# Performance work log

Hardware: AMD Instinct MI355X
Metric: run time of the kernel (lower is better)

The kernel has to match this reference:

```python
import jax, jax.numpy as jnp
import numpy as np
from jax import lax

GAMMA = 0.99

def setup_inputs() -> dict:
    key = jax.random.key(0)
    ks = jax.random.split(key, 6)
    B, T, D = 2048, 512, 16
    return {
        "Q": jax.random.normal(ks[0], (B, T, D), dtype=jnp.float32),
        "expected_target_Q": jax.random.normal(ks[1], (B, T, D), dtype=jnp.float32),
        "target_Q": jax.random.normal(ks[2], (B, T, D), dtype=jnp.float32),
        "rewards": jax.random.normal(ks[3], (B, T, D), dtype=jnp.float32),
        "target_policy_probs": jax.random.normal(ks[4], (B, T, D), dtype=jnp.float32),
        "behaviour_policy_probs": jax.random.normal(ks[5], (B, T), dtype=jnp.float32),
    }


def _q_ret(expected_target_Q, target_Q, rewards, target_policy_probs, behaviour_policy_probs):
    # importance weights c = exp(min(log_pi - log_b, 0)), shape [B, T, D]
    c = jnp.exp(jnp.minimum(target_policy_probs - behaviour_policy_probs[..., None], 0.0))
    T = target_Q.shape[1]
    # time-major slices for steps j = 0..T-2
    tm = lambda x: jnp.swapaxes(x, 0, 1)  # [T, B, D] -> scan over leading axis
    xs = (tm(rewards[:, : T - 1]), tm(expected_target_Q[:, 1:]),
          tm(c[:, 1:]), tm(target_Q[:, 1:]))

    def step(carry, x):
        r, e, cw, tq = x
        q = r + GAMMA * (e + cw * (carry - tq))
        return q, q

    # reverse scan: Q_ret[j] depends on Q_ret[j+1]; init carry is target_Q[:, -1]
    _, q_ret = lax.scan(step, target_Q[:, -1], xs, reverse=True)
    return jnp.swapaxes(q_ret, 0, 1)  # [B, T-1, D] == Q_ret[:, :-1]


def reference(Q, expected_target_Q, target_Q, rewards, target_policy_probs, behaviour_policy_probs):
    q_ret = lax.stop_gradient(
        _q_ret(expected_target_Q, target_Q, rewards, target_policy_probs, behaviour_policy_probs))
    return jnp.mean((Q[:, :-1] - q_ret) ** 2)
```

## Files before the change

kernel.cpp:

```cpp
#include <hip/hip_runtime.h>


constexpr int B = 2048;
constexpr int T = 512;
constexpr int D = 16;
constexpr float GAMMA = 0.99f;

__global__ __launch_bounds__(64) void retrace_kernel(
    const float* __restrict__ Q,
    const float* __restrict__ eQ,
    const float* __restrict__ tQ,
    const float* __restrict__ rw,
    const float* __restrict__ tpp,
    const float* __restrict__ bpp,
    float* __restrict__ out)
{
    const int tid = blockIdx.x * blockDim.x + threadIdx.x;
    const int b = tid >> 4;
    const int d = tid & 15;

    const size_t base = (size_t)b * T * D + d;
    const float* __restrict__ q_p = Q   + base;
    const float* __restrict__ e_p = eQ  + base;
    const float* __restrict__ t_p = tQ  + base;
    const float* __restrict__ r_p = rw  + base;
    const float* __restrict__ p_p = tpp + base;
    const float* __restrict__ b_p = bpp + (size_t)b * T;

    float carry = t_p[(size_t)(T - 1) * D];
    float acc = 0.0f;

    #pragma unroll 8
    for (int j = T - 2; j >= 0; --j) {
        const float diff = p_p[(size_t)(j + 1) * D] - b_p[j + 1];
        const float cw   = __builtin_exp2f(fminf(diff, 0.0f) * 1.44269504088896340736f);
        const float tqv  = t_p[(size_t)(j + 1) * D];
        const float ev   = e_p[(size_t)(j + 1) * D];
        const float rv   = r_p[(size_t)j * D];
        const float qv   = q_p[(size_t)j * D];

        const float q = fmaf(GAMMA, fmaf(cw, carry - tqv, ev), rv);
        const float err = qv - q;
        acc = fmaf(err, err, acc);
        carry = q;
    }

    #pragma unroll
    for (int off = 32; off > 0; off >>= 1)
        acc += __shfl_down(acc, off, 64);

    if (threadIdx.x == 0) {
        constexpr float inv_count = 1.0f / ((float)B * (float)(T - 1) * (float)D);
        atomicAdd(out, acc * inv_count);
    }
}

extern "C" void kernel_launch(void* const* d_in, const int* in_sizes, int n_in,
                              void* d_out, int out_size, void* d_ws, size_t ws_size,
                              hipStream_t stream) {
    const float* Q   = (const float*)d_in[0];
    const float* eQ  = (const float*)d_in[1];
    const float* tQ  = (const float*)d_in[2];
    const float* rw  = (const float*)d_in[3];
    const float* tpp = (const float*)d_in[4];
    const float* bpp = (const float*)d_in[5];
    float* out = (float*)d_out;

    hipMemsetAsync(out, 0, sizeof(float), stream);

    retrace_kernel<<<dim3(512), dim3(64), 0, stream>>>(Q, eQ, tQ, rw, tpp, bpp, out);
}
```

Before: 333.6 us.

## Parallelize reverse scan over time chunks with affine carry composition

Splits the time axis into 16 chunks of 32 steps. Each chunk computes its affine carry map (alpha, beta) plus partial sums that make the squared-error loss a quadratic in the unknown incoming carry. A second small kernel walks the chunks in reverse, applies the carry and sums the loss exactly. Loads are widened to float4 with four features per thread. The old kernel ran only 512 wavefronts, each through a 511-step serial chain, so the GPU was badly underfilled. The cost is a workspace round trip, a second launch, and possible floating-point reassociation error from expanding the square.

```diff
diff --git a/kernel.cpp b/kernel.cpp
--- a/kernel.cpp
+++ b/kernel.cpp
@@ -4,47 +4,120 @@
 constexpr int B = 2048;
 constexpr int T = 512;
 constexpr int D = 16;
+constexpr int NC = 16;
+constexpr int CS = 32;
+constexpr int SQ = B * (D / 4);
 constexpr float GAMMA = 0.99f;
+constexpr float LOG2E = 1.44269504088896340736f;
 
-__global__ __launch_bounds__(64) void retrace_kernel(
+__global__ __launch_bounds__(256) void retrace_phase1(
     const float* __restrict__ Q,
     const float* __restrict__ eQ,
     const float* __restrict__ tQ,
     const float* __restrict__ rw,
     const float* __restrict__ tpp,
     const float* __restrict__ bpp,
+    float4* __restrict__ ws)
+{
+    const int s  = blockIdx.x * blockDim.x + threadIdx.x;
+    const int k  = blockIdx.y;
+    const int b  = s >> 2;
+    const int dq = s & 3;
+
+    const int j_start = k * CS;
+    const int j_end   = min(j_start + CS, T - 1);
+
+    const float4* __restrict__ q4 = (const float4*)Q;
+    const float4* __restrict__ e4 = (const float4*)eQ;
+    const float4* __restrict__ t4 = (const float4*)tQ;
+    const float4* __restrict__ r4 = (const float4*)rw;
+    const float4* __restrict__ p4 = (const float4*)tpp;
+    const size_t row = (size_t)b * T * 4 + dq;
+    const float* __restrict__ b_p = bpp + (size_t)b * T;
+
+    float alpha[4] = {0.f, 0.f, 0.f, 0.f};
+    float beta[4]  = {1.f, 1.f, 1.f, 1.f};
+    float P[4] = {0.f, 0.f, 0.f, 0.f};
+    float S[4] = {0.f, 0.f, 0.f, 0.f};
+    float W[4] = {0.f, 0.f, 0.f, 0.f};
+
+    #pragma unroll 4
+    for (int j = j_end - 1; j >= j_start; --j) {
+        const float4 tp4 = p4[row + (size_t)(j + 1) * 4];
+        const float4 tq4 = t4[row + (size_t)(j + 1) * 4];
+        const float4 ee4 = e4[row + (size_t)(j + 1) * 4];
+        const float4 rr4 = r4[row + (size_t)j * 4];
+        const float4 qq4 = q4[row + (size_t)j * 4];
+        const float  bp  = b_p[j + 1];
+
+        const float* tp = (const float*)&tp4;
+        const float* tq = (const float*)&tq4;
+        const float* ee = (const float*)&ee4;
+        const float* rr = (const float*)&rr4;
+        const float* qq = (const float*)&qq4;
+
+        #pragma unroll
+        for (int i = 0; i < 4; ++i) {
+            const float cw = __builtin_exp2f(fminf(tp[i] - bp, 0.f) * LOG2E);
+            const float g  = GAMMA * cw;
+            const float base = fmaf(-g, tq[i], fmaf(GAMMA, ee[i], rr[i]));
+            alpha[i] = fmaf(g, alpha[i], base);
+            beta[i]  = g * beta[i];
+            const float u = qq[i] - alpha[i];
+            P[i] = fmaf(u, u, P[i]);
+            S[i] = fmaf(u, beta[i], S[i]);
+            W[i] = fmaf(beta[i], beta[i], W[i]);
+        }
+    }
+
+    const size_t o = (size_t)k * SQ + s;
+    float4* wsA = ws;
+    float4* wsM = ws + (size_t)NC * SQ;
+    float4* wsP = ws + (size_t)2 * NC * SQ;
+    float4* wsS = ws + (size_t)3 * NC * SQ;
+    float4* wsW = ws + (size_t)4 * NC * SQ;
+    wsA[o] = *(const float4*)alpha;
+    wsM[o] = *(const float4*)beta;
+    wsP[o] = *(const float4*)P;
+    wsS[o] = *(const float4*)S;
+    wsW[o] = *(const float4*)W;
+}
+
+__global__ __launch_bounds__(64) void retrace_phase2(
+    const float* __restrict__ tQ,
+    const float4* __restrict__ ws,
     float* __restrict__ out)
 {
-    const int tid = blockIdx.x * blockDim.x + threadIdx.x;
-    const int b = tid >> 4;
-    const int d = tid & 15;
+    const int s  = blockIdx.x * blockDim.x + threadIdx.x;
+    const int b  = s >> 2;
+    const int dq = s & 3;
 
-    const size_t base = (size_t)b * T * D + d;
-    const float* __restrict__ q_p = Q   + base;
-    const float* __restrict__ e_p = eQ  + base;
-    const float* __restrict__ t_p = tQ  + base;
-    const float* __restrict__ r_p = rw  + base;
-    const float* __restrict__ p_p = tpp + base;
-    const float* __restrict__ b_p = bpp + (size_t)b * T;
+    const float4* wsA = ws;
+    const float4* wsM = ws + (size_t)NC * SQ;
+    const float4* wsP = ws + (size_t)2 * NC * SQ;
+    const float4* wsS = ws + (size_t)3 * NC * SQ;
+    const float4* wsW = ws + (size_t)4 * NC * SQ;
 
-    float carry = t_p[(size_t)(T - 1) * D];
-    float acc = 0.0f;
+    float4 c4 = ((const float4*)tQ)[((size_t)b * T + (T - 1)) * 4 + dq];
+    float* c = (float*)&c4;
+    float loss[4] = {0.f, 0.f, 0.f, 0.f};
 
-    #pragma unroll 8
-    for (int j = T - 2; j >= 0; --j) {
-        const float diff = p_p[(size_t)(j + 1) * D] - b_p[j + 1];
-        const float cw   = __builtin_exp2f(fminf(diff, 0.0f) * 1.44269504088896340736f);
-        const float tqv  = t_p[(size_t)(j + 1) * D];
-        const float ev   = e_p[(size_t)(j + 1) * D];
-        const float rv   = r_p[(size_t)j * D];
-        const float qv   = q_p[(size_t)j * D];
-
-        const float q = fmaf(GAMMA, fmaf(cw, carry - tqv, ev), rv);
-        const float err = qv - q;
-        acc = fmaf(err, err, acc);
-        carry = q;
+    for (int k = NC - 1; k >= 0; --k) {
+        const size_t o = (size_t)k * SQ + s;
+        const float4 A4 = wsA[o], M4 = wsM[o], P4 = wsP[o], S4 = wsS[o], W4 = wsW[o];
+        const float* A = (const float*)&A4;
+        const float* M = (const float*)&M4;
+        const float* P = (const float*)&P4;
+        const float* S = (const float*)&S4;
+        const float* W = (const float*)&W4;
+        #pragma unroll
+        for (int i = 0; i < 4; ++i) {
+            loss[i] += fmaf(c[i], fmaf(W[i], c[i], -2.f * S[i]), P[i]);
+            c[i] = fmaf(M[i], c[i], A[i]);
+        }
     }
 
+    float acc = (loss[0] + loss[1]) + (loss[2] + loss[3]);
     #pragma unroll
     for (int off = 32; off > 0; off >>= 1)
         acc += __shfl_down(acc, off, 64);
@@ -65,8 +138,12 @@
     const float* tpp = (const float*)d_in[4];
     const float* bpp = (const float*)d_in[5];
     float* out = (float*)d_out;
+    float4* ws = (float4*)d_ws;
 
     hipMemsetAsync(out, 0, sizeof(float), stream);
 
-    retrace_kernel<<<dim3(512), dim3(64), 0, stream>>>(Q, eQ, tQ, rw, tpp, bpp, out);
+    retrace_phase1<<<dim3(SQ / 256, NC), dim3(256), 0, stream>>>(
+        Q, eQ, tQ, rw, tpp, bpp, ws);
+
+    retrace_phase2<<<dim3(SQ / 64), dim3(64), 0, stream>>>(tQ, ws, out);
 }
```

New measurement: 320.0 us. 1.04x faster.
